# Optimization experiments

Measured on AMD Instinct MI355X. Metric: run time of the kernel, lower is better.

## Reference

```python
import jax, jax.numpy as jnp
import numpy as np

FP8_MAX = 448.0  # max finite value of float8_e4m3fn

def _quant_fp8(v):
    # round to fp8_e4m3fn grid, keep values in fp32 (simulates fp8 storage)
    return v.astype(jnp.float8_e4m3fn).astype(jnp.float32)

def setup_inputs() -> dict:
    key = jax.random.key(0)
    k1, k2, k3 = jax.random.split(key, 3)
    M, K, N = 4096, 4096, 16384  # tokens, input_size, output_size
    x = jax.random.normal(k1, (M, K), dtype=jnp.float32)
    # build a per-output-channel (per_Token quant of the weight) fp8 weight
    w = jax.random.normal(k2, (N, K), dtype=jnp.float32) * 0.02
    weight_scale = jnp.max(jnp.abs(w), axis=1, keepdims=True) / FP8_MAX  # [N,1] fp32
    weight = _quant_fp8(w / weight_scale)  # fp8 codes stored as fp32
    bias = jax.random.normal(k3, (N,), dtype=jnp.float32) * 0.01
    return {"x": x, "weight": weight, "weight_scale": weight_scale, "bias": bias}

def reference(x, weight, weight_scale, bias):
    # --- dynamic per-token quantization of the activations (x_scale is None path) ---
    x_scale = jnp.max(jnp.abs(x), axis=-1, keepdims=True) / FP8_MAX  # [M,1]
    x_scale = jnp.maximum(x_scale, 1e-12)
    xq = _quant_fp8(x / x_scale)  # fp8 activation codes
    # --- a8w8 GEMM with fp32 accumulation, fused dequant + bias ---
    y = jnp.einsum('mk,nk->mn', xq, weight)          # [M,N] fp32 accum
    y = y * x_scale * weight_scale.T + bias          # per-token * per-channel dequant
    return y
```

## Files before the change

### kernel.cpp

```cpp
#include <hip/hip_runtime.h>

#define M_DIM 4096
#define K_DIM 4096
#define N_DIM 16384

typedef float v4f __attribute__((ext_vector_type(4)));
typedef __attribute__((address_space(3))) unsigned char lds_uchar;

__global__ __launch_bounds__(256) void quant_x_kernel(
    const float* __restrict__ x, unsigned char* __restrict__ xq,
    float* __restrict__ xs) {
  const int row = blockIdx.x;
  const int t = threadIdx.x;
  const float4* xr4 = (const float4*)(x + (size_t)row * K_DIM);

  float4 v[4];
  float am = 0.f;
#pragma unroll
  for (int i = 0; i < 4; ++i) {
    v[i] = xr4[t + 256 * i];
    am = fmaxf(am, fmaxf(fmaxf(fabsf(v[i].x), fabsf(v[i].y)),
                         fmaxf(fabsf(v[i].z), fabsf(v[i].w))));
  }
#pragma unroll
  for (int off = 32; off > 0; off >>= 1)
    am = fmaxf(am, __shfl_xor(am, off, 64));
  __shared__ float red[4];
  if ((t & 63) == 0) red[t >> 6] = am;
  __syncthreads();
  am = fmaxf(fmaxf(red[0], red[1]), fmaxf(red[2], red[3]));

  const float scale = fmaxf(am / 448.0f, 1e-12f);
  if (t == 0) xs[row] = scale;

  uint32_t* out = (uint32_t*)(xq + (size_t)row * K_DIM);
#pragma unroll
  for (int i = 0; i < 4; ++i) {
    float a0 = v[i].x / scale, a1 = v[i].y / scale;
    float a2 = v[i].z / scale, a3 = v[i].w / scale;
    uint32_t p = __builtin_amdgcn_cvt_pk_fp8_f32(a0, a1, 0, false);
    p = __builtin_amdgcn_cvt_pk_fp8_f32(a2, a3, p, true);
    out[t + 256 * i] = p;
  }
}

__global__ __launch_bounds__(256) void quant_w_kernel(
    const float4* __restrict__ w, uint32_t* __restrict__ wq) {
  const int i = blockIdx.x * 256 + threadIdx.x;
  float4 v = w[i];
  uint32_t p = __builtin_amdgcn_cvt_pk_fp8_f32(v.x, v.y, 0, false);
  p = __builtin_amdgcn_cvt_pk_fp8_f32(v.z, v.w, p, true);
  wq[i] = p;
}

__device__ __forceinline__ void async_copy16(const void* g, void* l) {
  __builtin_amdgcn_global_load_lds(
      (const __attribute__((address_space(1))) void*)g,
      (__attribute__((address_space(3))) void*)l, 16, 0, 0);
}

__device__ __forceinline__ long long lds_read_b64(const lds_uchar* p) {
  long long d;
  asm volatile("ds_read_b64 %0, %1" : "=v"(d) : "v"(p));
  return d;
}

#define MF(a, b, c) __builtin_amdgcn_mfma_f32_16x16x32_fp8_fp8(a, b, c, 0, 0, 0)

#define AOFF(i, ks) ((ks) ? (aoff[i] ^ 32u) : aoff[i])
#define BOFF(j, ks) ((ks) ? (boff[j] ^ 32u) : boff[j])

#define PHASE(ks, mh, STAGE_STMT, TAIL_STMT)                            \
  {                                                                     \
    fa0 = lds_read_b64(bb + AOFF(4 * (mh) + 0, ks));                    \
    fa1 = lds_read_b64(bb + AOFF(4 * (mh) + 1, ks));                    \
    fa2 = lds_read_b64(bb + AOFF(4 * (mh) + 2, ks));                    \
    fa3 = lds_read_b64(bb + AOFF(4 * (mh) + 3, ks));                    \
    if ((mh) == 0) {                                                    \
      fb0 = lds_read_b64(bb + BOFF(0, ks));                             \
      fb1 = lds_read_b64(bb + BOFF(1, ks));                             \
      fb2 = lds_read_b64(bb + BOFF(2, ks));                             \
      fb3 = lds_read_b64(bb + BOFF(3, ks));                             \
    }                                                                   \
    STAGE_STMT;                                                         \
    __builtin_amdgcn_s_barrier();                                       \
    asm volatile("s_waitcnt lgkmcnt(0)");                               \
    __builtin_amdgcn_sched_barrier(0);                                  \
    __builtin_amdgcn_s_setprio(1);                                      \
    acc[4 * (mh) + 0][0] = MF(fa0, fb0, acc[4 * (mh) + 0][0]);          \
    acc[4 * (mh) + 0][1] = MF(fa0, fb1, acc[4 * (mh) + 0][1]);          \
    acc[4 * (mh) + 0][2] = MF(fa0, fb2, acc[4 * (mh) + 0][2]);          \
    acc[4 * (mh) + 0][3] = MF(fa0, fb3, acc[4 * (mh) + 0][3]);          \
    acc[4 * (mh) + 1][0] = MF(fa1, fb0, acc[4 * (mh) + 1][0]);          \
    acc[4 * (mh) + 1][1] = MF(fa1, fb1, acc[4 * (mh) + 1][1]);          \
    acc[4 * (mh) + 1][2] = MF(fa1, fb2, acc[4 * (mh) + 1][2]);          \
    acc[4 * (mh) + 1][3] = MF(fa1, fb3, acc[4 * (mh) + 1][3]);          \
    acc[4 * (mh) + 2][0] = MF(fa2, fb0, acc[4 * (mh) + 2][0]);          \
    acc[4 * (mh) + 2][1] = MF(fa2, fb1, acc[4 * (mh) + 2][1]);          \
    acc[4 * (mh) + 2][2] = MF(fa2, fb2, acc[4 * (mh) + 2][2]);          \
    acc[4 * (mh) + 2][3] = MF(fa2, fb3, acc[4 * (mh) + 2][3]);          \
    acc[4 * (mh) + 3][0] = MF(fa3, fb0, acc[4 * (mh) + 3][0]);          \
    acc[4 * (mh) + 3][1] = MF(fa3, fb1, acc[4 * (mh) + 3][1]);          \
    acc[4 * (mh) + 3][2] = MF(fa3, fb2, acc[4 * (mh) + 3][2]);          \
    acc[4 * (mh) + 3][3] = MF(fa3, fb3, acc[4 * (mh) + 3][3]);          \
    __builtin_amdgcn_sched_barrier(0);                                  \
    __builtin_amdgcn_s_setprio(0);                                      \
    TAIL_STMT;                                                          \
    __builtin_amdgcn_s_barrier();                                       \
  }

#define TILE(DO_STAGE, TAIL_STMT)                                       \
  PHASE(0, 0, if (DO_STAGE) async_copy16(gA0 + kst, sd), (void)0)       \
  PHASE(0, 1, if (DO_STAGE) async_copy16(gA1 + kst, sd + 8192), (void)0)\
  PHASE(1, 0, if (DO_STAGE) async_copy16(gB0 + kst, sd + 16384), (void)0)\
  PHASE(1, 1, if (DO_STAGE) async_copy16(gB1 + kst, sd + 24576), TAIL_STMT)

__global__ __launch_bounds__(512, 2) void gemm_fp8_kernel(
    const unsigned char* __restrict__ Aq,
    const unsigned char* __restrict__ Bq,
    const float* __restrict__ xs,
    const float* __restrict__ wscale,
    const float* __restrict__ bias,
    float* __restrict__ y) {
  constexpr int BK = 64;
  __shared__ __align__(16) unsigned char smem[3 * 32768];

  const int tid = threadIdx.x;

  const int id = blockIdx.x;
  const int sw = (id & 7) * 128 + (id >> 3);
  const int bm = (sw >> 6) * 256;
  const int bn = (sw & 63) * 256;

  const int srow = tid >> 2;
  const unsigned scol = (unsigned)(((tid & 3) ^ ((srow >> 1) & 3)) * 16);
  const unsigned char* gA0 = Aq + (size_t)(bm + srow) * K_DIM + scol;
  const unsigned char* gA1 = gA0 + (size_t)128 * K_DIM;
  const unsigned char* gB0 = Bq + (size_t)(bn + srow) * K_DIM + scol;
  const unsigned char* gB1 = gB0 + (size_t)128 * K_DIM;

  const int lane = tid & 63;
  const int w = tid >> 6;
  const int wmo = (w >> 2) * 128;
  const int wno = (w & 3) * 64;
  const int lrow = lane & 15;
  const int lq = lane >> 4;
  const unsigned xm = (unsigned)(((lrow >> 1) & 3) << 4);
  const unsigned koff0 = ((unsigned)(lq * 8)) ^ xm;

  unsigned aoff[8], boff[4];
#pragma unroll
  for (int i = 0; i < 8; ++i)
    aoff[i] = (unsigned)((wmo + i * 16 + lrow) * 64) + koff0;
#pragma unroll
  for (int j = 0; j < 4; ++j)
    boff[j] = 16384u + (unsigned)((wno + j * 16 + lrow) * 64) + koff0;

  v4f acc[8][4];
#pragma unroll
  for (int i = 0; i < 8; ++i)
#pragma unroll
    for (int j = 0; j < 4; ++j) acc[i][j] = {0.f, 0.f, 0.f, 0.f};

  long long fa0, fa1, fa2, fa3;
  long long fb0 = 0, fb1 = 0, fb2 = 0, fb3 = 0;

  {
    unsigned char* s0 = smem + tid * 16;
    async_copy16(gA0, s0);
    async_copy16(gA1, s0 + 8192);
    async_copy16(gB0, s0 + 16384);
    async_copy16(gB1, s0 + 24576);
    unsigned char* s1 = s0 + 32768;
    async_copy16(gA0 + BK, s1);
    async_copy16(gA1 + BK, s1 + 8192);
    async_copy16(gB0 + BK, s1 + 16384);
    async_copy16(gB1 + BK, s1 + 24576);
  }
  asm volatile("s_waitcnt vmcnt(4)");
  __builtin_amdgcn_s_barrier();

  int cur = 0, stg = 2;
  for (int t = 0; t < 62; ++t) {
    const lds_uchar* bb = (const lds_uchar*)(smem + cur * 32768);
    unsigned char* sd = smem + stg * 32768 + tid * 16;
    const int kst = (t + 2) * BK;
    TILE(1, asm volatile("s_waitcnt vmcnt(4)"))
    cur = (cur == 2) ? 0 : cur + 1;
    stg = (stg == 2) ? 0 : stg + 1;
  }
  {
    const lds_uchar* bb = (const lds_uchar*)(smem + cur * 32768);
    unsigned char* sd = smem + tid * 16;
    const int kst = 0;
    TILE(0, asm volatile("s_waitcnt vmcnt(0)"))
    cur = (cur == 2) ? 0 : cur + 1;
  }
  {
    const lds_uchar* bb = (const lds_uchar*)(smem + cur * 32768);
    unsigned char* sd = smem + tid * 16;
    const int kst = 0;
    TILE(0, (void)0)
  }

  const int bmw = bm + wmo;
  const int bnw = bn + wno;
  float xsv[8][4];
#pragma unroll
  for (int i = 0; i < 8; ++i)
#pragma unroll
    for (int r = 0; r < 4; ++r)
      xsv[i][r] = xs[bmw + i * 16 + lq * 4 + r];

#pragma unroll
  for (int j = 0; j < 4; ++j) {
    const int col = bnw + j * 16 + lrow;
    const float wsc = wscale[col];
    const float bv = bias[col];
#pragma unroll
    for (int i = 0; i < 8; ++i) {
      const int row0 = bmw + i * 16 + lq * 4;
#pragma unroll
      for (int r = 0; r < 4; ++r)
        y[(size_t)(row0 + r) * N_DIM + col] =
            acc[i][j][r] * xsv[i][r] * wsc + bv;
    }
  }
}

extern "C" void kernel_launch(void* const* d_in, const int* in_sizes, int n_in,
                              void* d_out, int out_size, void* d_ws,
                              size_t ws_size, hipStream_t stream) {
  const float* x = (const float*)d_in[0];
  const float* w = (const float*)d_in[1];
  const float* wscale = (const float*)d_in[2];
  const float* bias = (const float*)d_in[3];
  float* y = (float*)d_out;

  unsigned char* xq = (unsigned char*)d_ws;
  unsigned char* wq = xq + (size_t)M_DIM * K_DIM;
  float* xs = (float*)(wq + (size_t)N_DIM * K_DIM);

  quant_x_kernel<<<M_DIM, 256, 0, stream>>>(x, xq, xs);
  quant_w_kernel<<<((size_t)N_DIM * K_DIM / 4) / 256, 256, 0, stream>>>(
      (const float4*)w, (uint32_t*)wq);
  gemm_fp8_kernel<<<(M_DIM / 256) * (N_DIM / 256), 512, 0, stream>>>(
      xq, wq, xs, wscale, bias, y);
}
```

Before: 842.3 us.

## Software-pipeline LDS fragment reads one phase ahead of MFMA issue

Restructures the inner K-loop so LDS fragment reads for the next phase (and the next tile's first phase) are issued before the current phase's MFMAs. It uses double-buffered register fragments and partial lgkmcnt waits in place of a full drain each phase. The goal is to hide LDS read latency behind matrix-core work. In exchange it uses more VGPRs for fragments and depends on carefully tuned vmcnt/lgkmcnt counts, where an error would give wrong results or lost occupancy.

```diff
diff --git a/kernel.cpp b/kernel.cpp
--- a/kernel.cpp
+++ b/kernel.cpp
@@ -67,53 +67,74 @@
 
 #define MF(a, b, c) __builtin_amdgcn_mfma_f32_16x16x32_fp8_fp8(a, b, c, 0, 0, 0)
 
-#define AOFF(i, ks) ((ks) ? (aoff[i] ^ 32u) : aoff[i])
-#define BOFF(j, ks) ((ks) ? (boff[j] ^ 32u) : boff[j])
-
-#define PHASE(ks, mh, STAGE_STMT, TAIL_STMT)                            \
-  {                                                                     \
-    fa0 = lds_read_b64(bb + AOFF(4 * (mh) + 0, ks));                    \
-    fa1 = lds_read_b64(bb + AOFF(4 * (mh) + 1, ks));                    \
-    fa2 = lds_read_b64(bb + AOFF(4 * (mh) + 2, ks));                    \
-    fa3 = lds_read_b64(bb + AOFF(4 * (mh) + 3, ks));                    \
-    if ((mh) == 0) {                                                    \
-      fb0 = lds_read_b64(bb + BOFF(0, ks));                             \
-      fb1 = lds_read_b64(bb + BOFF(1, ks));                             \
-      fb2 = lds_read_b64(bb + BOFF(2, ks));                             \
-      fb3 = lds_read_b64(bb + BOFF(3, ks));                             \
-    }                                                                   \
-    STAGE_STMT;                                                         \
-    __builtin_amdgcn_s_barrier();                                       \
-    asm volatile("s_waitcnt lgkmcnt(0)");                               \
-    __builtin_amdgcn_sched_barrier(0);                                  \
-    __builtin_amdgcn_s_setprio(1);                                      \
-    acc[4 * (mh) + 0][0] = MF(fa0, fb0, acc[4 * (mh) + 0][0]);          \
-    acc[4 * (mh) + 0][1] = MF(fa0, fb1, acc[4 * (mh) + 0][1]);          \
-    acc[4 * (mh) + 0][2] = MF(fa0, fb2, acc[4 * (mh) + 0][2]);          \
-    acc[4 * (mh) + 0][3] = MF(fa0, fb3, acc[4 * (mh) + 0][3]);          \
-    acc[4 * (mh) + 1][0] = MF(fa1, fb0, acc[4 * (mh) + 1][0]);          \
-    acc[4 * (mh) + 1][1] = MF(fa1, fb1, acc[4 * (mh) + 1][1]);          \
-    acc[4 * (mh) + 1][2] = MF(fa1, fb2, acc[4 * (mh) + 1][2]);          \
-    acc[4 * (mh) + 1][3] = MF(fa1, fb3, acc[4 * (mh) + 1][3]);          \
-    acc[4 * (mh) + 2][0] = MF(fa2, fb0, acc[4 * (mh) + 2][0]);          \
-    acc[4 * (mh) + 2][1] = MF(fa2, fb1, acc[4 * (mh) + 2][1]);          \
-    acc[4 * (mh) + 2][2] = MF(fa2, fb2, acc[4 * (mh) + 2][2]);          \
-    acc[4 * (mh) + 2][3] = MF(fa2, fb3, acc[4 * (mh) + 2][3]);          \
-    acc[4 * (mh) + 3][0] = MF(fa3, fb0, acc[4 * (mh) + 3][0]);          \
-    acc[4 * (mh) + 3][1] = MF(fa3, fb1, acc[4 * (mh) + 3][1]);          \
-    acc[4 * (mh) + 3][2] = MF(fa3, fb2, acc[4 * (mh) + 3][2]);          \
-    acc[4 * (mh) + 3][3] = MF(fa3, fb3, acc[4 * (mh) + 3][3]);          \
-    __builtin_amdgcn_sched_barrier(0);                                  \
-    __builtin_amdgcn_s_setprio(0);                                      \
-    TAIL_STMT;                                                          \
-    __builtin_amdgcn_s_barrier();                                       \
-  }
-
-#define TILE(DO_STAGE, TAIL_STMT)                                       \
-  PHASE(0, 0, if (DO_STAGE) async_copy16(gA0 + kst, sd), (void)0)       \
-  PHASE(0, 1, if (DO_STAGE) async_copy16(gA1 + kst, sd + 8192), (void)0)\
-  PHASE(1, 0, if (DO_STAGE) async_copy16(gB0 + kst, sd + 16384), (void)0)\
-  PHASE(1, 1, if (DO_STAGE) async_copy16(gB1 + kst, sd + 24576), TAIL_STMT)
+#define MFMA16(R, A0, A1, A2, A3, B)                     \
+  acc[(R) + 0][0] = MF(A0, B##0, acc[(R) + 0][0]);       \
+  acc[(R) + 0][1] = MF(A0, B##1, acc[(R) + 0][1]);       \
+  acc[(R) + 0][2] = MF(A0, B##2, acc[(R) + 0][2]);       \
+  acc[(R) + 0][3] = MF(A0, B##3, acc[(R) + 0][3]);       \
+  acc[(R) + 1][0] = MF(A1, B##0, acc[(R) + 1][0]);       \
+  acc[(R) + 1][1] = MF(A1, B##1, acc[(R) + 1][1]);       \
+  acc[(R) + 1][2] = MF(A1, B##2, acc[(R) + 1][2]);       \
+  acc[(R) + 1][3] = MF(A1, B##3, acc[(R) + 1][3]);       \
+  acc[(R) + 2][0] = MF(A2, B##0, acc[(R) + 2][0]);       \
+  acc[(R) + 2][1] = MF(A2, B##1, acc[(R) + 2][1]);       \
+  acc[(R) + 2][2] = MF(A2, B##2, acc[(R) + 2][2]);       \
+  acc[(R) + 2][3] = MF(A2, B##3, acc[(R) + 2][3]);       \
+  acc[(R) + 3][0] = MF(A3, B##0, acc[(R) + 3][0]);       \
+  acc[(R) + 3][1] = MF(A3, B##1, acc[(R) + 3][1]);       \
+  acc[(R) + 3][2] = MF(A3, B##2, acc[(R) + 3][2]);       \
+  acc[(R) + 3][3] = MF(A3, B##3, acc[(R) + 3][3])
+
+#define PH_CORE(LGKMSTR, R, A0, A1, A2, A3, B, TAIL)     \
+  __builtin_amdgcn_s_barrier();                          \
+  asm volatile("s_waitcnt lgkmcnt(" LGKMSTR ")");        \
+  __builtin_amdgcn_sched_barrier(0);                     \
+  __builtin_amdgcn_s_setprio(1);                         \
+  MFMA16(R, A0, A1, A2, A3, B);                          \
+  __builtin_amdgcn_sched_barrier(0);                     \
+  __builtin_amdgcn_s_setprio(0);                         \
+  TAIL;                                                  \
+  __builtin_amdgcn_s_barrier();
+
+#define TILE4(S, P2TAIL, DO_NEXT, P3LGKM)                \
+         \
+  a1_0 = lds_read_b64(bufC + aoff[4]);                   \
+  a1_1 = lds_read_b64(bufC + aoff[5]);                   \
+  a1_2 = lds_read_b64(bufC + aoff[6]);                   \
+  a1_3 = lds_read_b64(bufC + aoff[7]);                   \
+  if (S) async_copy16(gA0 + kst, sd);                    \
+  PH_CORE("4", 0, a0_0, a0_1, a0_2, a0_3, b0_, ;)        \
+  \
+  a0_0 = lds_read_b64(bufC + (aoff[0] ^ 32u));           \
+  a0_1 = lds_read_b64(bufC + (aoff[1] ^ 32u));           \
+  a0_2 = lds_read_b64(bufC + (aoff[2] ^ 32u));           \
+  a0_3 = lds_read_b64(bufC + (aoff[3] ^ 32u));           \
+  b1_0 = lds_read_b64(bufC + (boff[0] ^ 32u));           \
+  b1_1 = lds_read_b64(bufC + (boff[1] ^ 32u));           \
+  b1_2 = lds_read_b64(bufC + (boff[2] ^ 32u));           \
+  b1_3 = lds_read_b64(bufC + (boff[3] ^ 32u));           \
+  if (S) async_copy16(gA1 + kst, sd + 8192);             \
+  PH_CORE("8", 4, a1_0, a1_1, a1_2, a1_3, b0_, ;)        \
+         \
+  a1_0 = lds_read_b64(bufC + (aoff[4] ^ 32u));           \
+  a1_1 = lds_read_b64(bufC + (aoff[5] ^ 32u));           \
+  a1_2 = lds_read_b64(bufC + (aoff[6] ^ 32u));           \
+  a1_3 = lds_read_b64(bufC + (aoff[7] ^ 32u));           \
+  if (S) async_copy16(gB0 + kst, sd + 16384);            \
+  PH_CORE("4", 0, a0_0, a0_1, a0_2, a0_3, b1_, P2TAIL)   \
+   \
+  if (DO_NEXT) {                                         \
+    a0_0 = lds_read_b64(bufN + aoff[0]);                 \
+    a0_1 = lds_read_b64(bufN + aoff[1]);                 \
+    a0_2 = lds_read_b64(bufN + aoff[2]);                 \
+    a0_3 = lds_read_b64(bufN + aoff[3]);                 \
+    b0_0 = lds_read_b64(bufN + boff[0]);                 \
+    b0_1 = lds_read_b64(bufN + boff[1]);                 \
+    b0_2 = lds_read_b64(bufN + boff[2]);                 \
+    b0_3 = lds_read_b64(bufN + boff[3]);                 \
+  }                                                      \
+  if (S) async_copy16(gB1 + kst, sd + 24576);            \
+  PH_CORE(P3LGKM, 4, a1_0, a1_1, a1_2, a1_3, b1_, ;)
 
 __global__ __launch_bounds__(512, 2) void gemm_fp8_kernel(
     const unsigned char* __restrict__ Aq,
@@ -162,8 +183,10 @@
 #pragma unroll
     for (int j = 0; j < 4; ++j) acc[i][j] = {0.f, 0.f, 0.f, 0.f};
 
-  long long fa0, fa1, fa2, fa3;
-  long long fb0 = 0, fb1 = 0, fb2 = 0, fb3 = 0;
+  long long a0_0, a0_1, a0_2, a0_3;
+  long long a1_0, a1_1, a1_2, a1_3;
+  long long b0_0, b0_1, b0_2, b0_3;
+  long long b1_0, b1_1, b1_2, b1_3;
 
   {
     unsigned char* s0 = smem + tid * 16;
@@ -180,27 +203,44 @@
   asm volatile("s_waitcnt vmcnt(4)");
   __builtin_amdgcn_s_barrier();
 
+  {
+    const lds_uchar* b0p = (const lds_uchar*)smem;
+    a0_0 = lds_read_b64(b0p + aoff[0]);
+    a0_1 = lds_read_b64(b0p + aoff[1]);
+    a0_2 = lds_read_b64(b0p + aoff[2]);
+    a0_3 = lds_read_b64(b0p + aoff[3]);
+    b0_0 = lds_read_b64(b0p + boff[0]);
+    b0_1 = lds_read_b64(b0p + boff[1]);
+    b0_2 = lds_read_b64(b0p + boff[2]);
+    b0_3 = lds_read_b64(b0p + boff[3]);
+  }
+
   int cur = 0, stg = 2;
   for (int t = 0; t < 62; ++t) {
-    const lds_uchar* bb = (const lds_uchar*)(smem + cur * 32768);
+    const int nxt = (cur == 2) ? 0 : cur + 1;
+    const lds_uchar* bufC = (const lds_uchar*)(smem + cur * 32768);
+    const lds_uchar* bufN = (const lds_uchar*)(smem + nxt * 32768);
     unsigned char* sd = smem + stg * 32768 + tid * 16;
     const int kst = (t + 2) * BK;
-    TILE(1, asm volatile("s_waitcnt vmcnt(4)"))
-    cur = (cur == 2) ? 0 : cur + 1;
+    TILE4(1, asm volatile("s_waitcnt vmcnt(3)"), 1, "8")
+    cur = nxt;
     stg = (stg == 2) ? 0 : stg + 1;
   }
   {
-    const lds_uchar* bb = (const lds_uchar*)(smem + cur * 32768);
+    const int nxt = (cur == 2) ? 0 : cur + 1;
+    const lds_uchar* bufC = (const lds_uchar*)(smem + cur * 32768);
+    const lds_uchar* bufN = (const lds_uchar*)(smem + nxt * 32768);
     unsigned char* sd = smem + tid * 16;
     const int kst = 0;
-    TILE(0, asm volatile("s_waitcnt vmcnt(0)"))
-    cur = (cur == 2) ? 0 : cur + 1;
-  }
-  {
-    const lds_uchar* bb = (const lds_uchar*)(smem + cur * 32768);
+    TILE4(0, asm volatile("s_waitcnt vmcnt(0)"), 1, "8")
+    cur = nxt;
+  }
+  {
+    const lds_uchar* bufC = (const lds_uchar*)(smem + cur * 32768);
+    const lds_uchar* bufN = bufC;
     unsigned char* sd = smem + tid * 16;
     const int kst = 0;
-    TILE(0, (void)0)
+    TILE4(0, ;, 0, "0")
   }
 
   const int bmw = bm + wmo;
```

Result: no change. 837.2 us (-0.6%).

## Restructure fp8 GEMM main loop into two phases with prefetched LDS fragments

Applied to the files above, without the earlier changes.

Replaces the four-phase-per-tile schedule (16 MFMAs per phase, LDS reads waited on fully before each phase) with two 32-MFMA phases per tile. The fragment reads for the next half-tile, and for the next buffer, are issued before the current MFMAs, so partial lgkmcnt waits let LDS reads overlap matrix math. Global staging is regrouped into two pairs per tile with a vmcnt(2) wait. It halves the barrier count per tile but doubles the fragment registers held per wave, which raises register pressure under launch_bounds(512,2).

```diff
diff --git a/kernel.cpp b/kernel.cpp
--- a/kernel.cpp
+++ b/kernel.cpp
@@ -67,53 +67,70 @@
 
 #define MF(a, b, c) __builtin_amdgcn_mfma_f32_16x16x32_fp8_fp8(a, b, c, 0, 0, 0)
 
-#define AOFF(i, ks) ((ks) ? (aoff[i] ^ 32u) : aoff[i])
-#define BOFF(j, ks) ((ks) ? (boff[j] ^ 32u) : boff[j])
-
-#define PHASE(ks, mh, STAGE_STMT, TAIL_STMT)                            \
-  {                                                                     \
-    fa0 = lds_read_b64(bb + AOFF(4 * (mh) + 0, ks));                    \
-    fa1 = lds_read_b64(bb + AOFF(4 * (mh) + 1, ks));                    \
-    fa2 = lds_read_b64(bb + AOFF(4 * (mh) + 2, ks));                    \
-    fa3 = lds_read_b64(bb + AOFF(4 * (mh) + 3, ks));                    \
-    if ((mh) == 0) {                                                    \
-      fb0 = lds_read_b64(bb + BOFF(0, ks));                             \
-      fb1 = lds_read_b64(bb + BOFF(1, ks));                             \
-      fb2 = lds_read_b64(bb + BOFF(2, ks));                             \
-      fb3 = lds_read_b64(bb + BOFF(3, ks));                             \
-    }                                                                   \
-    STAGE_STMT;                                                         \
-    __builtin_amdgcn_s_barrier();                                       \
-    asm volatile("s_waitcnt lgkmcnt(0)");                               \
-    __builtin_amdgcn_sched_barrier(0);                                  \
-    __builtin_amdgcn_s_setprio(1);                                      \
-    acc[4 * (mh) + 0][0] = MF(fa0, fb0, acc[4 * (mh) + 0][0]);          \
-    acc[4 * (mh) + 0][1] = MF(fa0, fb1, acc[4 * (mh) + 0][1]);          \
-    acc[4 * (mh) + 0][2] = MF(fa0, fb2, acc[4 * (mh) + 0][2]);          \
-    acc[4 * (mh) + 0][3] = MF(fa0, fb3, acc[4 * (mh) + 0][3]);          \
-    acc[4 * (mh) + 1][0] = MF(fa1, fb0, acc[4 * (mh) + 1][0]);          \
-    acc[4 * (mh) + 1][1] = MF(fa1, fb1, acc[4 * (mh) + 1][1]);          \
-    acc[4 * (mh) + 1][2] = MF(fa1, fb2, acc[4 * (mh) + 1][2]);          \
-    acc[4 * (mh) + 1][3] = MF(fa1, fb3, acc[4 * (mh) + 1][3]);          \
-    acc[4 * (mh) + 2][0] = MF(fa2, fb0, acc[4 * (mh) + 2][0]);          \
-    acc[4 * (mh) + 2][1] = MF(fa2, fb1, acc[4 * (mh) + 2][1]);          \
-    acc[4 * (mh) + 2][2] = MF(fa2, fb2, acc[4 * (mh) + 2][2]);          \
-    acc[4 * (mh) + 2][3] = MF(fa2, fb3, acc[4 * (mh) + 2][3]);          \
-    acc[4 * (mh) + 3][0] = MF(fa3, fb0, acc[4 * (mh) + 3][0]);          \
-    acc[4 * (mh) + 3][1] = MF(fa3, fb1, acc[4 * (mh) + 3][1]);          \
-    acc[4 * (mh) + 3][2] = MF(fa3, fb2, acc[4 * (mh) + 3][2]);          \
-    acc[4 * (mh) + 3][3] = MF(fa3, fb3, acc[4 * (mh) + 3][3]);          \
-    __builtin_amdgcn_sched_barrier(0);                                  \
-    __builtin_amdgcn_s_setprio(0);                                      \
-    TAIL_STMT;                                                          \
-    __builtin_amdgcn_s_barrier();                                       \
-  }
-
-#define TILE(DO_STAGE, TAIL_STMT)                                       \
-  PHASE(0, 0, if (DO_STAGE) async_copy16(gA0 + kst, sd), (void)0)       \
-  PHASE(0, 1, if (DO_STAGE) async_copy16(gA1 + kst, sd + 8192), (void)0)\
-  PHASE(1, 0, if (DO_STAGE) async_copy16(gB0 + kst, sd + 16384), (void)0)\
-  PHASE(1, 1, if (DO_STAGE) async_copy16(gB1 + kst, sd + 24576), TAIL_STMT)
+#define MROW(I, AI, B)                       \
+  acc[I][0] = MF(AI, B##0, acc[I][0]);       \
+  acc[I][1] = MF(AI, B##1, acc[I][1]);       \
+  acc[I][2] = MF(AI, B##2, acc[I][2]);       \
+  acc[I][3] = MF(AI, B##3, acc[I][3]);
+
+#define MFMA32(A, B)                         \
+  MROW(0, A##0, B) MROW(1, A##1, B)          \
+  MROW(2, A##2, B) MROW(3, A##3, B)          \
+  MROW(4, A##4, B) MROW(5, A##5, B)          \
+  MROW(6, A##6, B) MROW(7, A##7, B)
+
+#define RD_X(BUF)                            \
+  ax0 = lds_read_b64(BUF + aoff[0]);         \
+  ax1 = lds_read_b64(BUF + aoff[1]);         \
+  ax2 = lds_read_b64(BUF + aoff[2]);         \
+  ax3 = lds_read_b64(BUF + aoff[3]);         \
+  ax4 = lds_read_b64(BUF + aoff[4]);         \
+  ax5 = lds_read_b64(BUF + aoff[5]);         \
+  ax6 = lds_read_b64(BUF + aoff[6]);         \
+  ax7 = lds_read_b64(BUF + aoff[7]);         \
+  bx0 = lds_read_b64(BUF + boff[0]);         \
+  bx1 = lds_read_b64(BUF + boff[1]);         \
+  bx2 = lds_read_b64(BUF + boff[2]);         \
+  bx3 = lds_read_b64(BUF + boff[3]);
+
+#define RD_Y(BUF)                            \
+  ay0 = lds_read_b64(BUF + (aoff[0] ^ 32u)); \
+  ay1 = lds_read_b64(BUF + (aoff[1] ^ 32u)); \
+  ay2 = lds_read_b64(BUF + (aoff[2] ^ 32u)); \
+  ay3 = lds_read_b64(BUF + (aoff[3] ^ 32u)); \
+  ay4 = lds_read_b64(BUF + (aoff[4] ^ 32u)); \
+  ay5 = lds_read_b64(BUF + (aoff[5] ^ 32u)); \
+  ay6 = lds_read_b64(BUF + (aoff[6] ^ 32u)); \
+  ay7 = lds_read_b64(BUF + (aoff[7] ^ 32u)); \
+  by0 = lds_read_b64(BUF + (boff[0] ^ 32u)); \
+  by1 = lds_read_b64(BUF + (boff[1] ^ 32u)); \
+  by2 = lds_read_b64(BUF + (boff[2] ^ 32u)); \
+  by3 = lds_read_b64(BUF + (boff[3] ^ 32u));
+
+#define PH2(LGK, A, B, TAIL)                      \
+  __builtin_amdgcn_s_barrier();                   \
+  asm volatile("s_waitcnt lgkmcnt(" LGK ")");     \
+  __builtin_amdgcn_sched_barrier(0);              \
+  __builtin_amdgcn_s_setprio(1);                  \
+  MFMA32(A, B);                                   \
+  __builtin_amdgcn_sched_barrier(0);              \
+  __builtin_amdgcn_s_setprio(0);                  \
+  TAIL;                                           \
+  __builtin_amdgcn_s_barrier();
+
+#define TILE2(S, DO_NEXT, PATAIL, PBLGK)               \
+  RD_Y(bufC)                                           \
+  if (S) {                                             \
+    async_copy16(gA0 + kst, sd);                       \
+    async_copy16(gA1 + kst, sd + 8192);                \
+  }                                                    \
+  PH2("12", ax, bx, PATAIL)                            \
+  if (DO_NEXT) { RD_X(bufN) }                          \
+  if (S) {                                             \
+    async_copy16(gB0 + kst, sd + 16384);               \
+    async_copy16(gB1 + kst, sd + 24576);               \
+  }                                                    \
+  PH2(PBLGK, ay, by, ;)
 
 __global__ __launch_bounds__(512, 2) void gemm_fp8_kernel(
     const unsigned char* __restrict__ Aq,
@@ -162,8 +179,10 @@
 #pragma unroll
     for (int j = 0; j < 4; ++j) acc[i][j] = {0.f, 0.f, 0.f, 0.f};
 
-  long long fa0, fa1, fa2, fa3;
-  long long fb0 = 0, fb1 = 0, fb2 = 0, fb3 = 0;
+  long long ax0, ax1, ax2, ax3, ax4, ax5, ax6, ax7;
+  long long bx0, bx1, bx2, bx3;
+  long long ay0, ay1, ay2, ay3, ay4, ay5, ay6, ay7;
+  long long by0, by1, by2, by3;
 
   {
     unsigned char* s0 = smem + tid * 16;
@@ -180,27 +199,37 @@
   asm volatile("s_waitcnt vmcnt(4)");
   __builtin_amdgcn_s_barrier();
 
+  {
+    const lds_uchar* b0p = (const lds_uchar*)smem;
+    RD_X(b0p)
+  }
+
   int cur = 0, stg = 2;
   for (int t = 0; t < 62; ++t) {
-    const lds_uchar* bb = (const lds_uchar*)(smem + cur * 32768);
+    const int nxt = (cur == 2) ? 0 : cur + 1;
+    const lds_uchar* bufC = (const lds_uchar*)(smem + cur * 32768);
+    const lds_uchar* bufN = (const lds_uchar*)(smem + nxt * 32768);
     unsigned char* sd = smem + stg * 32768 + tid * 16;
     const int kst = (t + 2) * BK;
-    TILE(1, asm volatile("s_waitcnt vmcnt(4)"))
-    cur = (cur == 2) ? 0 : cur + 1;
+    TILE2(1, 1, asm volatile("s_waitcnt vmcnt(2)"), "12")
+    cur = nxt;
     stg = (stg == 2) ? 0 : stg + 1;
   }
   {
-    const lds_uchar* bb = (const lds_uchar*)(smem + cur * 32768);
+    const int nxt = (cur == 2) ? 0 : cur + 1;
+    const lds_uchar* bufC = (const lds_uchar*)(smem + cur * 32768);
+    const lds_uchar* bufN = (const lds_uchar*)(smem + nxt * 32768);
     unsigned char* sd = smem + tid * 16;
     const int kst = 0;
-    TILE(0, asm volatile("s_waitcnt vmcnt(0)"))
-    cur = (cur == 2) ? 0 : cur + 1;
-  }
-  {
-    const lds_uchar* bb = (const lds_uchar*)(smem + cur * 32768);
+    TILE2(0, 1, asm volatile("s_waitcnt vmcnt(0)"), "12")
+    cur = nxt;
+  }
+  {
+    const lds_uchar* bufC = (const lds_uchar*)(smem + cur * 32768);
+    const lds_uchar* bufN = bufC;
     unsigned char* sd = smem + tid * 16;
     const int kst = 0;
-    TILE(0, (void)0)
+    TILE2(0, 0, ;, "0")
   }
 
   const int bmw = bm + wmo;
```

New measurement: 841.7 us. No clear change (-0.1%).
